# Performance work log

Measured on AMD Instinct MI355X. Metric: run time of the kernel, lower is better.

Reference implementation:

```python
import jax, jax.numpy as jnp
import numpy as np

H = 128  # hidden size

def lstm_layer(x, Wih, Whh, bih, bhh):
    """One PyTorch-semantics LSTM layer. x: (B,T,F). Gate order: i,f,g,o."""
    B = x.shape[0]
    # Precompute input contributions for all timesteps: (B,T,4H)
    xg = jnp.einsum('btf,gf->btg', x, Wih) + bih + bhh
    def step(carry, xt):
        h, c = carry
        g = xt + h @ Whh.T                      # (B,4H)
        i, f, gg, o = jnp.split(g, 4, axis=-1)
        i = jax.nn.sigmoid(i)
        f = jax.nn.sigmoid(f)
        gg = jnp.tanh(gg)
        o = jax.nn.sigmoid(o)
        c = f * c + i * gg
        h = o * jnp.tanh(c)
        return (h, c), h
    h0 = jnp.zeros((B, H), x.dtype)
    (hT, cT), hs = jax.lax.scan(step, (h0, h0), jnp.swapaxes(xg, 0, 1))
    return jnp.swapaxes(hs, 0, 1), hT  # (B,T,H), (B,H)


def setup_inputs() -> dict:
    key = jax.random.key(0)
    ks = jax.random.split(key, 20)
    B, T = 256, 2048
    s = 1.0 / np.sqrt(H)  # PyTorch default init scale
    inp = {
        'x': jax.random.normal(ks[0], (B, T, 1), jnp.float32),
        'Wih0': jax.random.uniform(ks[1], (4 * H, 1), jnp.float32, -s, s),
        'Whh0': jax.random.uniform(ks[2], (4 * H, H), jnp.float32, -s, s),
        'bih0': jax.random.uniform(ks[3], (4 * H,), jnp.float32, -s, s),
        'bhh0': jax.random.uniform(ks[4], (4 * H,), jnp.float32, -s, s),
        'Wih1': jax.random.uniform(ks[5], (4 * H, H), jnp.float32, -s, s),
        'Whh1': jax.random.uniform(ks[6], (4 * H, H), jnp.float32, -s, s),
        'bih1': jax.random.uniform(ks[7], (4 * H,), jnp.float32, -s, s),
        'bhh1': jax.random.uniform(ks[8], (4 * H,), jnp.float32, -s, s),
        'Wih2': jax.random.uniform(ks[9], (4 * H, H), jnp.float32, -s, s),
        'Whh2': jax.random.uniform(ks[10], (4 * H, H), jnp.float32, -s, s),
        'bih2': jax.random.uniform(ks[11], (4 * H,), jnp.float32, -s, s),
        'bhh2': jax.random.uniform(ks[12], (4 * H,), jnp.float32, -s, s),
        'fc1_w': jax.random.uniform(ks[13], (64, H), jnp.float32, -s, s),
        'fc1_b': jax.random.uniform(ks[14], (64,), jnp.float32, -s, s),
        'fc2_w': jax.random.uniform(ks[15], (5, 64), jnp.float32, -1.0 / 8, 1.0 / 8),
        'fc2_b': jax.random.uniform(ks[16], (5,), jnp.float32, -1.0 / 8, 1.0 / 8),
    }
    return inp


def reference(x, Wih0, Whh0, bih0, bhh0, Wih1, Whh1, bih1, bhh1,
              Wih2, Whh2, bih2, bhh2, fc1_w, fc1_b, fc2_w, fc2_b):
    # 3-layer LSTM (eval mode: inter-layer dropout is identity)
    h1, _ = lstm_layer(x, Wih0, Whh0, bih0, bhh0)
    h2, _ = lstm_layer(h1, Wih1, Whh1, bih1, bhh1)
    _, hT = lstm_layer(h2, Wih2, Whh2, bih2, bhh2)  # hn[-1]: (B,H)
    z = jax.nn.relu(hT @ fc1_w.T + fc1_b)
    return z @ fc2_w.T + fc2_b  # (B, num_classes)
```

## Files before the change

kernel.cpp:

```cpp
#include <hip/hip_runtime.h>

#define HDIM 128
#define TDIM 2048
#define BDIM 256
#define CHUNK 16
#define NT 512
#define XGP 20

typedef _Float16 half8_t __attribute__((ext_vector_type(8)));
typedef float f32x4 __attribute__((ext_vector_type(4)));

__device__ __forceinline__ f32x4 mfma16(half8_t a, half8_t b, f32x4 c) {
    return __builtin_amdgcn_mfma_f32_16x16x32_f16(a, b, c, 0, 0, 0);
}

__device__ __forceinline__ void fast_barrier() {
    asm volatile("s_waitcnt lgkmcnt(0)\n\ts_barrier" ::: "memory");
}

__device__ __forceinline__ float sigm_f(float x) { return 1.0f / (1.0f + __expf(-x)); }
__device__ __forceinline__ float tanh_f(float x) { return 1.0f - 2.0f / (1.0f + __expf(2.0f * x)); }

__global__ __launch_bounds__(256)
void convert_w(const float* __restrict__ Whh0, const float* __restrict__ Wih1,
               const float* __restrict__ Whh1, const float* __restrict__ Wih2,
               const float* __restrict__ Whh2, _Float16* __restrict__ dst) {
    int i = blockIdx.x * 256 + threadIdx.x;
    int seg = i >> 16, off = i & 65535;
    const float* s = (seg == 0) ? Whh0 : (seg == 1) ? Wih1 : (seg == 2) ? Whh1
                   : (seg == 3) ? Wih2 : Whh2;
    dst[i] = (_Float16)s[off];
}

__global__ __launch_bounds__(NT, 2)
void lstm3_kernel(const float* __restrict__ x,   const float* __restrict__ Wih0,
                  const float* __restrict__ bih0, const float* __restrict__ bhh0,
                  const float* __restrict__ bih1, const float* __restrict__ bhh1,
                  const float* __restrict__ bih2, const float* __restrict__ bhh2,
                  const float* __restrict__ fc1w, const float* __restrict__ fc1b,
                  const float* __restrict__ fc2w, const float* __restrict__ fc2b,
                  float* __restrict__ out,
                  _Float16* __restrict__ gbuf, const _Float16* __restrict__ wbuf)
{
    __shared__ __align__(16) _Float16 hwin_s[CHUNK][HDIM];
    __shared__ __align__(16) _Float16 xin_s[2][CHUNK][HDIM];
    __shared__ __align__(16) float xg_s[2][512 * XGP];
    __shared__ __align__(16) float z_s[64];

    const int tid = threadIdx.x;
    const int ln = tid & 63;
    const int wv = tid >> 6;
    const int n16 = ln & 15;
    const int kb = (ln >> 4) * 8;
    const int un = wv * 16 + n16;
    const int b = blockIdx.x;

    {
        float bsum[4], w0[4];
        half8_t bhh[4][4];
#pragma unroll
        for (int tau = 0; tau < 4; ++tau) {
            const int g = tau * HDIM + un;
            bsum[tau] = bih0[g] + bhh0[g];
            w0[tau] = Wih0[g];
#pragma unroll
            for (int kk = 0; kk < 4; ++kk)
                bhh[tau][kk] = *(const half8_t*)(wbuf + (size_t)g * HDIM + kk * 32 + kb);
        }
        if (tid < HDIM) hwin_s[CHUNK - 1][tid] = (_Float16)0.f;
        float c = 0.f;
        float4 xp[4];
        {
            const float4* xq = (const float4*)(x + (size_t)b * TDIM);
#pragma unroll
            for (int i = 0; i < 4; ++i) xp[i] = xq[i];
        }

#pragma unroll 1
        for (int t0 = 0; t0 < TDIM; t0 += CHUNK) {
            float xv[CHUNK];
#pragma unroll
            for (int i = 0; i < 4; ++i) {
                xv[4 * i] = xp[i].x; xv[4 * i + 1] = xp[i].y;
                xv[4 * i + 2] = xp[i].z; xv[4 * i + 3] = xp[i].w;
            }
            int tn = (t0 + CHUNK < TDIM) ? (t0 + CHUNK) : t0;
            const float4* xq = (const float4*)(x + (size_t)b * TDIM + tn);
#pragma unroll
            for (int i = 0; i < 4; ++i) xp[i] = xq[i];

#pragma unroll
            for (int tt = 0; tt < CHUNK; ++tt) {
                fast_barrier();
                const int t = t0 + tt, row = (t + CHUNK - 1) & 15;
                half8_t A0 = *(const half8_t*)&hwin_s[row][kb];
                half8_t A1 = *(const half8_t*)&hwin_s[row][32 + kb];
                half8_t A2 = *(const half8_t*)&hwin_s[row][64 + kb];
                half8_t A3 = *(const half8_t*)&hwin_s[row][96 + kb];
                float g4[4];
#pragma unroll
                for (int tau = 0; tau < 4; ++tau) {
                    f32x4 Cz = {0.f, 0.f, 0.f, 0.f};
                    Cz = mfma16(A0, bhh[tau][0], Cz);
                    Cz = mfma16(A1, bhh[tau][1], Cz);
                    Cz = mfma16(A2, bhh[tau][2], Cz);
                    Cz = mfma16(A3, bhh[tau][3], Cz);
                    g4[tau] = Cz[0];
                }
                float ig = sigm_f(g4[0] + xv[tt] * w0[0] + bsum[0]);
                float fg = sigm_f(g4[1] + xv[tt] * w0[1] + bsum[1]);
                float gg = tanh_f(g4[2] + xv[tt] * w0[2] + bsum[2]);
                float og = sigm_f(g4[3] + xv[tt] * w0[3] + bsum[3]);
                c = fg * c + ig * gg;
                if (kb == 0) hwin_s[t & 15][un] = (_Float16)(og * tanh_f(c));
            }
            fast_barrier();
            int2 v = ((const int2*)&hwin_s[0][0])[tid];
            ((int2*)(gbuf + ((size_t)b * TDIM + t0) * HDIM))[tid] = v;
        }
    }

#pragma unroll 1
    for (int layer = 1; layer < 3; ++layer) {
        const _Float16* whh_p = wbuf + (size_t)((layer == 1) ? 2 : 4) * 65536;
        const _Float16* wih_p = wbuf + (size_t)((layer == 1) ? 1 : 3) * 65536;
        const float* bih = (layer == 1) ? bih1 : bih2;
        const float* bhh = (layer == 1) ? bhh1 : bhh2;

        float bsum[4];
        half8_t bhhf[4][4], bihf[4][4];
#pragma unroll
        for (int tau = 0; tau < 4; ++tau) {
            const int g = tau * HDIM + un;
            bsum[tau] = bih[g] + bhh[g];
#pragma unroll
            for (int kk = 0; kk < 4; ++kk)
                bhhf[tau][kk] = *(const half8_t*)(whh_p + (size_t)g * HDIM + kk * 32 + kb);
            const int gp = (wv * 4 + tau) * 16 + n16;
#pragma unroll
            for (int kk = 0; kk < 4; ++kk)
                bihf[tau][kk] = *(const half8_t*)(wih_p + (size_t)gp * HDIM + kk * 32 + kb);
        }

        __syncthreads();
        if (tid < HDIM) hwin_s[CHUNK - 1][tid] = (_Float16)0.f;
        float c = 0.f;

        int2 stage = ((const int2*)(gbuf + (size_t)b * TDIM * HDIM))[tid];
        ((int2*)&xin_s[0][0][0])[tid] = stage;
        __syncthreads();
        {
            half8_t A0 = *(const half8_t*)&xin_s[0][n16][kb];
            half8_t A1 = *(const half8_t*)&xin_s[0][n16][32 + kb];
            half8_t A2 = *(const half8_t*)&xin_s[0][n16][64 + kb];
            half8_t A3 = *(const half8_t*)&xin_s[0][n16][96 + kb];
#pragma unroll
            for (int tau = 0; tau < 4; ++tau) {
                f32x4 a = {0.f, 0.f, 0.f, 0.f};
                a = mfma16(A0, bihf[tau][0], a);
                a = mfma16(A1, bihf[tau][1], a);
                a = mfma16(A2, bihf[tau][2], a);
                a = mfma16(A3, bihf[tau][3], a);
                const int g = (wv * 4 + tau) * 16 + n16;
                *(f32x4*)&xg_s[0][g * XGP + (kb >> 1)] = a;
            }
        }
        stage = ((const int2*)(gbuf + ((size_t)b * TDIM + CHUNK) * HDIM))[tid];

        f32x4 pacc[4];
#pragma unroll 1
        for (int t0 = 0; t0 < TDIM; t0 += CHUNK) {
            const int ci = t0 >> 4, rbuf = ci & 1, cb = rbuf ^ 1;
            ((int2*)&xin_s[cb][0][0])[tid] = stage;
            int tn = (t0 + 2 * CHUNK < TDIM) ? (t0 + 2 * CHUNK) : t0;
            stage = ((const int2*)(gbuf + ((size_t)b * TDIM + tn) * HDIM))[tid];

            float2 xgv[4];
#pragma unroll
            for (int tt = 0; tt < CHUNK; ++tt) {
                fast_barrier();
                const int t = t0 + tt, row = (t + CHUNK - 1) & 15;
                half8_t A0 = *(const half8_t*)&hwin_s[row][kb];
                half8_t A1 = *(const half8_t*)&hwin_s[row][32 + kb];
                half8_t A2 = *(const half8_t*)&hwin_s[row][64 + kb];
                half8_t A3 = *(const half8_t*)&hwin_s[row][96 + kb];

                if (tt == 0) {
                    half8_t X0 = *(const half8_t*)&xin_s[cb][n16][kb];
                    half8_t X1 = *(const half8_t*)&xin_s[cb][n16][32 + kb];
                    half8_t X2 = *(const half8_t*)&xin_s[cb][n16][64 + kb];
                    half8_t X3 = *(const half8_t*)&xin_s[cb][n16][96 + kb];
#pragma unroll
                    for (int tau = 0; tau < 4; ++tau) {
                        f32x4 a = {0.f, 0.f, 0.f, 0.f};
                        a = mfma16(X0, bihf[tau][0], a);
                        a = mfma16(X1, bihf[tau][1], a);
                        a = mfma16(X2, bihf[tau][2], a);
                        a = mfma16(X3, bihf[tau][3], a);
                        pacc[tau] = a;
                    }
                }
                if ((tt & 1) == 0) {
#pragma unroll
                    for (int q = 0; q < 4; ++q)
                        xgv[q] = *(const float2*)&xg_s[rbuf][(q * HDIM + un) * XGP + tt];
                }

                float g4[4];
#pragma unroll
                for (int tau = 0; tau < 4; ++tau) {
                    f32x4 Cz = {0.f, 0.f, 0.f, 0.f};
                    Cz = mfma16(A0, bhhf[tau][0], Cz);
                    Cz = mfma16(A1, bhhf[tau][1], Cz);
                    Cz = mfma16(A2, bhhf[tau][2], Cz);
                    Cz = mfma16(A3, bhhf[tau][3], Cz);
                    g4[tau] = Cz[0];
                }

                float x0 = (tt & 1) ? xgv[0].y : xgv[0].x;
                float x1 = (tt & 1) ? xgv[1].y : xgv[1].x;
                float x2 = (tt & 1) ? xgv[2].y : xgv[2].x;
                float x3 = (tt & 1) ? xgv[3].y : xgv[3].x;
                float ig = sigm_f(g4[0] + x0 + bsum[0]);
                float fg = sigm_f(g4[1] + x1 + bsum[1]);
                float gg = tanh_f(g4[2] + x2 + bsum[2]);
                float og = sigm_f(g4[3] + x3 + bsum[3]);
                c = fg * c + ig * gg;
                if (kb == 0) hwin_s[t & 15][un] = (_Float16)(og * tanh_f(c));

                if (tt == CHUNK - 1) {
#pragma unroll
                    for (int tau = 0; tau < 4; ++tau) {
                        const int g = (wv * 4 + tau) * 16 + n16;
                        *(f32x4*)&xg_s[cb][g * XGP + (kb >> 1)] = pacc[tau];
                    }
                }
            }
            if (layer == 1) {
                fast_barrier();
                int2 v = ((const int2*)&hwin_s[0][0])[tid];
                ((int2*)(gbuf + ((size_t)b * TDIM + t0) * HDIM))[tid] = v;
            }
        }
    }

    __syncthreads();
    if (tid < 64) {
        const float* w = fc1w + tid * HDIM;
        float s = fc1b[tid];
#pragma unroll
        for (int k = 0; k < HDIM; ++k) s += w[k] * (float)hwin_s[CHUNK - 1][k];
        z_s[tid] = fmaxf(s, 0.0f);
    }
    __syncthreads();
    if (tid < 5) {
        const float* w = fc2w + tid * 64;
        float s = fc2b[tid];
#pragma unroll
        for (int k = 0; k < 64; ++k) s += w[k] * z_s[k];
        out[b * 5 + tid] = s;
    }
}

extern "C" void kernel_launch(void* const* d_in, const int* in_sizes, int n_in,
                              void* d_out, int out_size, void* d_ws, size_t ws_size,
                              hipStream_t stream) {
    (void)in_sizes; (void)n_in; (void)out_size; (void)ws_size;
    const float* x    = (const float*)d_in[0];
    const float* Wih0 = (const float*)d_in[1];
    const float* Whh0 = (const float*)d_in[2];
    const float* bih0 = (const float*)d_in[3];
    const float* bhh0 = (const float*)d_in[4];
    const float* Wih1 = (const float*)d_in[5];
    const float* Whh1 = (const float*)d_in[6];
    const float* bih1 = (const float*)d_in[7];
    const float* bhh1 = (const float*)d_in[8];
    const float* Wih2 = (const float*)d_in[9];
    const float* Whh2 = (const float*)d_in[10];
    const float* bih2 = (const float*)d_in[11];
    const float* bhh2 = (const float*)d_in[12];
    const float* fc1w = (const float*)d_in[13];
    const float* fc1b = (const float*)d_in[14];
    const float* fc2w = (const float*)d_in[15];
    const float* fc2b = (const float*)d_in[16];
    float* out = (float*)d_out;

    _Float16* gbuf = (_Float16*)d_ws;
    _Float16* wbuf = gbuf + (size_t)67108864;

    hipLaunchKernelGGL(convert_w, dim3(1280), dim3(256), 0, stream,
                       Whh0, Wih1, Whh1, Wih2, Whh2, wbuf);
    hipLaunchKernelGGL(lstm3_kernel, dim3(BDIM), dim3(NT), 0, stream,
                       x, Wih0, bih0, bhh0, bih1, bhh1, bih2, bhh2,
                       fc1w, fc1b, fc2w, fc2b, out, gbuf, wbuf);
}
```

Measured before the change: 3.663 ms.

## Wavefront-pipeline all three LSTM layers in one time loop without global staging

Result: slower. 5.540 ms (+51.2%).

```diff
diff --git a/kernel.cpp b/kernel.cpp
--- a/kernel.cpp
+++ b/kernel.cpp
@@ -1,10 +1,10 @@
 #include <hip/hip_runtime.h>
+
 
 #define HDIM 128
 #define TDIM 2048
 #define BDIM 256
-#define CHUNK 16
-#define NT 512
+#define NT 256
 #define XGP 20
 
 typedef _Float16 half8_t __attribute__((ext_vector_type(8)));
@@ -17,9 +17,6 @@
 __device__ __forceinline__ void fast_barrier() {
     asm volatile("s_waitcnt lgkmcnt(0)\n\ts_barrier" ::: "memory");
 }
-
-__device__ __forceinline__ float sigm_f(float x) { return 1.0f / (1.0f + __expf(-x)); }
-__device__ __forceinline__ float tanh_f(float x) { return 1.0f - 2.0f / (1.0f + __expf(2.0f * x)); }
 
 __global__ __launch_bounds__(256)
 void convert_w(const float* __restrict__ Whh0, const float* __restrict__ Wih1,
@@ -32,233 +29,198 @@
     dst[i] = (_Float16)s[off];
 }
 
-__global__ __launch_bounds__(NT, 2)
+#define RECG(Lc, gc, A0_,A1_,A2_,A3_, selout_) { \
+    f32x4 z0 = {0.f,0.f,0.f,0.f}; f32x4 z1 = z0, z2 = z0, z3 = z0; \
+    z0 = mfma16(A0_, whf[Lc][gc][0][0], z0); \
+    z0 = mfma16(A1_, whf[Lc][gc][0][1], z0); \
+    z0 = mfma16(A2_, whf[Lc][gc][0][2], z0); \
+    z0 = mfma16(A3_, whf[Lc][gc][0][3], z0); \
+    z1 = mfma16(A0_, whf[Lc][gc][1][0], z1); \
+    z1 = mfma16(A1_, whf[Lc][gc][1][1], z1); \
+    z1 = mfma16(A2_, whf[Lc][gc][1][2], z1); \
+    z1 = mfma16(A3_, whf[Lc][gc][1][3], z1); \
+    z2 = mfma16(A0_, whf[Lc][gc][2][0], z2); \
+    z2 = mfma16(A1_, whf[Lc][gc][2][1], z2); \
+    z2 = mfma16(A2_, whf[Lc][gc][2][2], z2); \
+    z2 = mfma16(A3_, whf[Lc][gc][2][3], z2); \
+    z3 = mfma16(A0_, whf[Lc][gc][3][0], z3); \
+    z3 = mfma16(A1_, whf[Lc][gc][3][1], z3); \
+    z3 = mfma16(A2_, whf[Lc][gc][3][2], z3); \
+    z3 = mfma16(A3_, whf[Lc][gc][3][3], z3); \
+    float s0_ = qb1 ? z1[0] : z0[0]; \
+    float s1_ = qb1 ? z3[0] : z2[0]; \
+    selout_ = qb2 ? s1_ : s0_; }
+
+#define GATECOMB(pre_, cr_, hout_) { \
+    float e_ = __expf(me * (pre_)); \
+    float r_ = __builtin_amdgcn_rcpf(1.0f + e_); \
+    float a_ = fmaf(Bq, r_, Aq); \
+    float v_ = __shfl_xor(a_, 32); \
+    float p_ = a_ * v_;             \
+    float f_ = __shfl_xor(a_, 16);  \
+    float o_ = __shfl_xor(v_, 16);  \
+    (cr_) = fmaf(f_, (cr_), p_); \
+    float e2_ = __expf(2.0f * (cr_)); \
+    float tc_ = fmaf(-2.0f, __builtin_amdgcn_rcpf(1.0f + e2_), 1.0f); \
+    (hout_) = o_ * tc_; }
+
+#define STEPL(Lc, RP_, WP_, PRE0_, PRE1_) { \
+    const _Float16* rp_ = (RP_); \
+    half8_t A0_ = *(const half8_t*)(rp_ + kb); \
+    half8_t A1_ = *(const half8_t*)(rp_ + 32 + kb); \
+    half8_t A2_ = *(const half8_t*)(rp_ + 64 + kb); \
+    half8_t A3_ = *(const half8_t*)(rp_ + 96 + kb); \
+    { float sel_; RECG(Lc, 0, A0_,A1_,A2_,A3_, sel_); \
+      float h_; GATECOMB((PRE0_), cst[Lc][0], h_); \
+      if (q == 0) (WP_)[wv*32 + n16] = (_Float16)h_; } \
+    { float sel_; RECG(Lc, 1, A0_,A1_,A2_,A3_, sel_); \
+      float h_; GATECOMB((PRE1_), cst[Lc][1], h_); \
+      if (q == 0) (WP_)[wv*32 + 16 + n16] = (_Float16)h_; } }
+
+#define PROJ(XGI, HSRC, WIH) { \
+    const _Float16* hr_ = &(HSRC)[n16][0]; \
+    half8_t X0 = *(const half8_t*)(hr_ + kb); \
+    half8_t X1 = *(const half8_t*)(hr_ + 32 + kb); \
+    half8_t X2 = *(const half8_t*)(hr_ + 64 + kb); \
+    half8_t X3 = *(const half8_t*)(hr_ + 96 + kb); \
+    _Pragma("unroll 4") \
+    for (int j = 0; j < 8; ++j) { \
+      const int gp_ = (wv*8 + j)*16 + n16; \
+      const _Float16* wp_ = (WIH) + (size_t)gp_*HDIM + kb; \
+      half8_t B0 = *(const half8_t*)(wp_); \
+      half8_t B1 = *(const half8_t*)(wp_ + 32); \
+      half8_t B2 = *(const half8_t*)(wp_ + 64); \
+      half8_t B3 = *(const half8_t*)(wp_ + 96); \
+      f32x4 a_ = {0.f,0.f,0.f,0.f}; \
+      a_ = mfma16(X0, B0, a_); a_ = mfma16(X1, B1, a_); \
+      a_ = mfma16(X2, B2, a_); a_ = mfma16(X3, B3, a_); \
+      *(f32x4*)&xg_s[XGI][gp_*XGP + q*4] = a_; \
+    } }
+
+__global__ __launch_bounds__(NT, 1)
 void lstm3_kernel(const float* __restrict__ x,   const float* __restrict__ Wih0,
                   const float* __restrict__ bih0, const float* __restrict__ bhh0,
                   const float* __restrict__ bih1, const float* __restrict__ bhh1,
                   const float* __restrict__ bih2, const float* __restrict__ bhh2,
                   const float* __restrict__ fc1w, const float* __restrict__ fc1b,
                   const float* __restrict__ fc2w, const float* __restrict__ fc2b,
-                  float* __restrict__ out,
-                  _Float16* __restrict__ gbuf, const _Float16* __restrict__ wbuf)
+                  float* __restrict__ out, const _Float16* __restrict__ wbuf)
 {
-    __shared__ __align__(16) _Float16 hwin_s[CHUNK][HDIM];
-    __shared__ __align__(16) _Float16 xin_s[2][CHUNK][HDIM];
+    __shared__ __align__(16) _Float16 hw[3][2][16][HDIM];
     __shared__ __align__(16) float xg_s[2][512 * XGP];
-    __shared__ __align__(16) float z_s[64];
+    __shared__ float x_s[16];
+    __shared__ float z_s[64];
 
     const int tid = threadIdx.x;
-    const int ln = tid & 63;
-    const int wv = tid >> 6;
+    const int ln  = tid & 63;
+    const int wv  = tid >> 6;
     const int n16 = ln & 15;
-    const int kb = (ln >> 4) * 8;
-    const int un = wv * 16 + n16;
+    const int q   = ln >> 4;
+    const int kb  = q * 8;
+    const bool qb1 = q & 1, qb2 = q & 2;
     const int b = blockIdx.x;
 
+    { int* p = (int*)hw; for (int i = tid; i < 6144; i += NT) p[i] = 0; }
+
+    half8_t whf[3][2][4][4];
     {
-        float bsum[4], w0[4];
-        half8_t bhh[4][4];
-#pragma unroll
-        for (int tau = 0; tau < 4; ++tau) {
-            const int g = tau * HDIM + un;
-            bsum[tau] = bih0[g] + bhh0[g];
-            w0[tau] = Wih0[g];
-#pragma unroll
-            for (int kk = 0; kk < 4; ++kk)
-                bhh[tau][kk] = *(const half8_t*)(wbuf + (size_t)g * HDIM + kk * 32 + kb);
-        }
-        if (tid < HDIM) hwin_s[CHUNK - 1][tid] = (_Float16)0.f;
-        float c = 0.f;
-        float4 xp[4];
-        {
-            const float4* xq = (const float4*)(x + (size_t)b * TDIM);
-#pragma unroll
-            for (int i = 0; i < 4; ++i) xp[i] = xq[i];
-        }
+        const _Float16* wrec[3] = { wbuf, wbuf + (size_t)2*65536, wbuf + (size_t)4*65536 };
+#pragma unroll
+        for (int L = 0; L < 3; ++L)
+#pragma unroll
+            for (int g = 0; g < 2; ++g)
+#pragma unroll
+                for (int tau = 0; tau < 4; ++tau)
+#pragma unroll
+                    for (int kk = 0; kk < 4; ++kk)
+                        whf[L][g][tau][kk] = *(const half8_t*)(wrec[L]
+                            + (size_t)(tau*HDIM + wv*32 + g*16 + n16)*HDIM + kk*32 + kb);
+    }
+    const _Float16* wih1p = wbuf + (size_t)1*65536;
+    const _Float16* wih2p = wbuf + (size_t)3*65536;
+
+    float bsv[3][2]; float w0v[2];
+    {
+        const float* bihs[3] = {bih0, bih1, bih2};
+        const float* bhhs[3] = {bhh0, bhh1, bhh2};
+#pragma unroll
+        for (int L = 0; L < 3; ++L)
+#pragma unroll
+            for (int g = 0; g < 2; ++g) {
+                int gate = q*HDIM + wv*32 + g*16 + n16;
+                bsv[L][g] = bihs[L][gate] + bhhs[L][gate];
+            }
+#pragma unroll
+        for (int g = 0; g < 2; ++g) w0v[g] = Wih0[q*HDIM + wv*32 + g*16 + n16];
+    }
+
+    const float me = (q == 2) ? 2.0f : -1.0f;
+    const float Aq = (q == 2) ? 1.0f : 0.0f;
+    const float Bq = (q == 2) ? -2.0f : 1.0f;
+
+    const int xgb0 = (q*HDIM + wv*32 + n16) * XGP;
+    const int xgb1 = xgb0 + 16 * XGP;
+
+    float cst[3][2] = {{0.f,0.f},{0.f,0.f},{0.f,0.f}};
+    const float* xb = x + (size_t)b * TDIM;
 
 #pragma unroll 1
-        for (int t0 = 0; t0 < TDIM; t0 += CHUNK) {
-            float xv[CHUNK];
-#pragma unroll
-            for (int i = 0; i < 4; ++i) {
-                xv[4 * i] = xp[i].x; xv[4 * i + 1] = xp[i].y;
-                xv[4 * i + 2] = xp[i].z; xv[4 * i + 3] = xp[i].w;
-            }
-            int tn = (t0 + CHUNK < TDIM) ? (t0 + CHUNK) : t0;
-            const float4* xq = (const float4*)(x + (size_t)b * TDIM + tn);
-#pragma unroll
-            for (int i = 0; i < 4; ++i) xp[i] = xq[i];
-
-#pragma unroll
-            for (int tt = 0; tt < CHUNK; ++tt) {
-                fast_barrier();
-                const int t = t0 + tt, row = (t + CHUNK - 1) & 15;
-                half8_t A0 = *(const half8_t*)&hwin_s[row][kb];
-                half8_t A1 = *(const half8_t*)&hwin_s[row][32 + kb];
-                half8_t A2 = *(const half8_t*)&hwin_s[row][64 + kb];
-                half8_t A3 = *(const half8_t*)&hwin_s[row][96 + kb];
-                float g4[4];
-#pragma unroll
-                for (int tau = 0; tau < 4; ++tau) {
-                    f32x4 Cz = {0.f, 0.f, 0.f, 0.f};
-                    Cz = mfma16(A0, bhh[tau][0], Cz);
-                    Cz = mfma16(A1, bhh[tau][1], Cz);
-                    Cz = mfma16(A2, bhh[tau][2], Cz);
-                    Cz = mfma16(A3, bhh[tau][3], Cz);
-                    g4[tau] = Cz[0];
-                }
-                float ig = sigm_f(g4[0] + xv[tt] * w0[0] + bsum[0]);
-                float fg = sigm_f(g4[1] + xv[tt] * w0[1] + bsum[1]);
-                float gg = tanh_f(g4[2] + xv[tt] * w0[2] + bsum[2]);
-                float og = sigm_f(g4[3] + xv[tt] * w0[3] + bsum[3]);
-                c = fg * c + ig * gg;
-                if (kb == 0) hwin_s[t & 15][un] = (_Float16)(og * tanh_f(c));
-            }
-            fast_barrier();
-            int2 v = ((const int2*)&hwin_s[0][0])[tid];
-            ((int2*)(gbuf + ((size_t)b * TDIM + t0) * HDIM))[tid] = v;
-        }
-    }
+    for (int s = 0; s < 130; ++s) {
+        const int par = s & 1;
+        const bool act0 = (s < 128), act1 = (s >= 1) && (s < 129), act2 = (s >= 2);
+
+        fast_barrier();
+
+        if (act0 && tid < 16) x_s[tid] = xb[s*16 + tid];
+        if (act1) PROJ(0, hw[0][par^1], wih1p);
+        if (act2) PROJ(1, hw[1][par], wih2p);
+
+        fast_barrier();
 
 #pragma unroll 1
-    for (int layer = 1; layer < 3; ++layer) {
-        const _Float16* whh_p = wbuf + (size_t)((layer == 1) ? 2 : 4) * 65536;
-        const _Float16* wih_p = wbuf + (size_t)((layer == 1) ? 1 : 3) * 65536;
-        const float* bih = (layer == 1) ? bih1 : bih2;
-        const float* bhh = (layer == 1) ? bhh1 : bhh2;
-
-        float bsum[4];
-        half8_t bhhf[4][4], bihf[4][4];
-#pragma unroll
-        for (int tau = 0; tau < 4; ++tau) {
-            const int g = tau * HDIM + un;
-            bsum[tau] = bih[g] + bhh[g];
-#pragma unroll
-            for (int kk = 0; kk < 4; ++kk)
-                bhhf[tau][kk] = *(const half8_t*)(whh_p + (size_t)g * HDIM + kk * 32 + kb);
-            const int gp = (wv * 4 + tau) * 16 + n16;
-#pragma unroll
-            for (int kk = 0; kk < 4; ++kk)
-                bihf[tau][kk] = *(const half8_t*)(wih_p + (size_t)gp * HDIM + kk * 32 + kb);
-        }
-
-        __syncthreads();
-        if (tid < HDIM) hwin_s[CHUNK - 1][tid] = (_Float16)0.f;
-        float c = 0.f;
-
-        int2 stage = ((const int2*)(gbuf + (size_t)b * TDIM * HDIM))[tid];
-        ((int2*)&xin_s[0][0][0])[tid] = stage;
-        __syncthreads();
-        {
-            half8_t A0 = *(const half8_t*)&xin_s[0][n16][kb];
-            half8_t A1 = *(const half8_t*)&xin_s[0][n16][32 + kb];
-            half8_t A2 = *(const half8_t*)&xin_s[0][n16][64 + kb];
-            half8_t A3 = *(const half8_t*)&xin_s[0][n16][96 + kb];
-#pragma unroll
-            for (int tau = 0; tau < 4; ++tau) {
-                f32x4 a = {0.f, 0.f, 0.f, 0.f};
-                a = mfma16(A0, bihf[tau][0], a);
-                a = mfma16(A1, bihf[tau][1], a);
-                a = mfma16(A2, bihf[tau][2], a);
-                a = mfma16(A3, bihf[tau][3], a);
-                const int g = (wv * 4 + tau) * 16 + n16;
-                *(f32x4*)&xg_s[0][g * XGP + (kb >> 1)] = a;
+        for (int tt = 0; tt < 16; ++tt) {
+            if (tt) fast_barrier();
+            const _Float16* r0p = tt ? hw[0][par][tt-1]   : hw[0][par^1][15];
+            _Float16*       q0p = hw[0][par][tt];
+            const _Float16* r1p = tt ? hw[1][par^1][tt-1] : hw[1][par][15];
+            _Float16*       q1p = hw[1][par^1][tt];
+            const _Float16* r2p = tt ? hw[2][par][tt-1]   : hw[2][par^1][15];
+            _Float16*       q2p = hw[2][par][tt];
+            const float xt = x_s[tt];
+
+            if (act0 && act1 && act2) {
+                STEPL(0, r0p, q0p, sel_ + fmaf(xt, w0v[0], bsv[0][0]),
+                                   sel_ + fmaf(xt, w0v[1], bsv[0][1]));
+                STEPL(1, r1p, q1p, sel_ + xg_s[0][xgb0 + tt] + bsv[1][0],
+                                   sel_ + xg_s[0][xgb1 + tt] + bsv[1][1]);
+                STEPL(2, r2p, q2p, sel_ + xg_s[1][xgb0 + tt] + bsv[2][0],
+                                   sel_ + xg_s[1][xgb1 + tt] + bsv[2][1]);
+            } else {
+                if (act0) STEPL(0, r0p, q0p, sel_ + fmaf(xt, w0v[0], bsv[0][0]),
+                                             sel_ + fmaf(xt, w0v[1], bsv[0][1]));
+                if (act1) STEPL(1, r1p, q1p, sel_ + xg_s[0][xgb0 + tt] + bsv[1][0],
+                                             sel_ + xg_s[0][xgb1 + tt] + bsv[1][1]);
+                if (act2) STEPL(2, r2p, q2p, sel_ + xg_s[1][xgb0 + tt] + bsv[2][0],
+                                             sel_ + xg_s[1][xgb1 + tt] + bsv[2][1]);
             }
         }
-        stage = ((const int2*)(gbuf + ((size_t)b * TDIM + CHUNK) * HDIM))[tid];
-
-        f32x4 pacc[4];
-#pragma unroll 1
-        for (int t0 = 0; t0 < TDIM; t0 += CHUNK) {
-            const int ci = t0 >> 4, rbuf = ci & 1, cb = rbuf ^ 1;
-            ((int2*)&xin_s[cb][0][0])[tid] = stage;
-            int tn = (t0 + 2 * CHUNK < TDIM) ? (t0 + 2 * CHUNK) : t0;
-            stage = ((const int2*)(gbuf + ((size_t)b * TDIM + tn) * HDIM))[tid];
-
-            float2 xgv[4];
-#pragma unroll
-            for (int tt = 0; tt < CHUNK; ++tt) {
-                fast_barrier();
-                const int t = t0 + tt, row = (t + CHUNK - 1) & 15;
-                half8_t A0 = *(const half8_t*)&hwin_s[row][kb];
-                half8_t A1 = *(const half8_t*)&hwin_s[row][32 + kb];
-                half8_t A2 = *(const half8_t*)&hwin_s[row][64 + kb];
-                half8_t A3 = *(const half8_t*)&hwin_s[row][96 + kb];
-
-                if (tt == 0) {
-                    half8_t X0 = *(const half8_t*)&xin_s[cb][n16][kb];
-                    half8_t X1 = *(const half8_t*)&xin_s[cb][n16][32 + kb];
-                    half8_t X2 = *(const half8_t*)&xin_s[cb][n16][64 + kb];
-                    half8_t X3 = *(const half8_t*)&xin_s[cb][n16][96 + kb];
-#pragma unroll
-                    for (int tau = 0; tau < 4; ++tau) {
-                        f32x4 a = {0.f, 0.f, 0.f, 0.f};
-                        a = mfma16(X0, bihf[tau][0], a);
-                        a = mfma16(X1, bihf[tau][1], a);
-                        a = mfma16(X2, bihf[tau][2], a);
-                        a = mfma16(X3, bihf[tau][3], a);
-                        pacc[tau] = a;
-                    }
-                }
-                if ((tt & 1) == 0) {
-#pragma unroll
-                    for (int q = 0; q < 4; ++q)
-                        xgv[q] = *(const float2*)&xg_s[rbuf][(q * HDIM + un) * XGP + tt];
-                }
-
-                float g4[4];
-#pragma unroll
-                for (int tau = 0; tau < 4; ++tau) {
-                    f32x4 Cz = {0.f, 0.f, 0.f, 0.f};
-                    Cz = mfma16(A0, bhhf[tau][0], Cz);
-                    Cz = mfma16(A1, bhhf[tau][1], Cz);
-                    Cz = mfma16(A2, bhhf[tau][2], Cz);
-                    Cz = mfma16(A3, bhhf[tau][3], Cz);
-                    g4[tau] = Cz[0];
-                }
-
-                float x0 = (tt & 1) ? xgv[0].y : xgv[0].x;
-                float x1 = (tt & 1) ? xgv[1].y : xgv[1].x;
-                float x2 = (tt & 1) ? xgv[2].y : xgv[2].x;
-                float x3 = (tt & 1) ? xgv[3].y : xgv[3].x;
-                float ig = sigm_f(g4[0] + x0 + bsum[0]);
-                float fg = sigm_f(g4[1] + x1 + bsum[1]);
-                float gg = tanh_f(g4[2] + x2 + bsum[2]);
-                float og = sigm_f(g4[3] + x3 + bsum[3]);
-                c = fg * c + ig * gg;
-                if (kb == 0) hwin_s[t & 15][un] = (_Float16)(og * tanh_f(c));
-
-                if (tt == CHUNK - 1) {
-#pragma unroll
-                    for (int tau = 0; tau < 4; ++tau) {
-                        const int g = (wv * 4 + tau) * 16 + n16;
-                        *(f32x4*)&xg_s[cb][g * XGP + (kb >> 1)] = pacc[tau];
-                    }
-                }
-            }
-            if (layer == 1) {
-                fast_barrier();
-                int2 v = ((const int2*)&hwin_s[0][0])[tid];
-                ((int2*)(gbuf + ((size_t)b * TDIM + t0) * HDIM))[tid] = v;
-            }
-        }
-    }
-
-    __syncthreads();
+    }
+
+    fast_barrier();
     if (tid < 64) {
         const float* w = fc1w + tid * HDIM;
-        float s = fc1b[tid];
-#pragma unroll
-        for (int k = 0; k < HDIM; ++k) s += w[k] * (float)hwin_s[CHUNK - 1][k];
-        z_s[tid] = fmaxf(s, 0.0f);
+        float sacc = fc1b[tid];
+#pragma unroll
+        for (int k = 0; k < HDIM; ++k) sacc += w[k] * (float)hw[2][1][15][k];
+        z_s[tid] = fmaxf(sacc, 0.0f);
     }
     __syncthreads();
     if (tid < 5) {
         const float* w = fc2w + tid * 64;
-        float s = fc2b[tid];
-#pragma unroll
-        for (int k = 0; k < 64; ++k) s += w[k] * z_s[k];
-        out[b * 5 + tid] = s;
+        float sacc = fc2b[tid];
+#pragma unroll
+        for (int k = 0; k < 64; ++k) sacc += w[k] * z_s[k];
+        out[b * 5 + tid] = sacc;
     }
 }
 
@@ -285,12 +247,11 @@
     const float* fc2b = (const float*)d_in[16];
     float* out = (float*)d_out;
 
-    _Float16* gbuf = (_Float16*)d_ws;
-    _Float16* wbuf = gbuf + (size_t)67108864;
+    _Float16* wbuf = (_Float16*)d_ws;
 
     hipLaunchKernelGGL(convert_w, dim3(1280), dim3(256), 0, stream,
                        Whh0, Wih1, Whh1, Wih2, Whh2, wbuf);
     hipLaunchKernelGGL(lstm3_kernel, dim3(BDIM), dim3(NT), 0, stream,
                        x, Wih0, bih0, bhh0, bih1, bhh1, bih2, bhh2,
-                       fc1w, fc1b, fc2w, fc2b, out, gbuf, wbuf);
-}
+                       fc1w, fc1b, fc2w, fc2b, out, wbuf);
+}
```
